# Optimization experiments

Measured on AMD Instinct MI355X. Metric: run time of the kernel, lower is better.

Reference implementation:

```python
import jax, jax.numpy as jnp
import numpy as np

HF = 14            # qubits (hidden_features)
SPECTRUM = 3       # spectrum_layer (data re-uploading blocks)
NSTEPS = 2         # N outer iterations
SEL_L = 3          # StronglyEntanglingLayers depth per block (weights1[..., 3, HF, 3])
DIM = 2 ** HF
BN_EPS = 1e-5

# wire 0 = most-significant bit (PennyLane default.qubit convention)
_bits = ((np.arange(DIM)[:, None] >> (HF - 1 - np.arange(HF))[None, :]) & 1)  # (DIM, HF)
Z_SIGNS = (1.0 - 2.0 * _bits).astype(np.float32)      # +1 for |0>, -1 for |1>
RZ_SIGNS = -Z_SIGNS                                    # (2b-1): RZ phase sign per wire
# CZ ring sign vectors for ranges r=1..SEL_L: (-1)^{sum_j b_j * b_{(j+r)%HF}}
_cz = []
for r in range(1, SEL_L + 1):
    parity = (_bits * _bits[:, (np.arange(HF) + r) % HF]).sum(axis=1) % 2
    _cz.append((1.0 - 2.0 * parity).astype(np.float32))
CZ_SIGNS = np.stack(_cz)  # (SEL_L, DIM)


def _rot_matrix(phi, theta, omega):
    # Rot = RZ(omega) @ RY(theta) @ RZ(phi)
    c = jnp.cos(theta / 2)
    s = jnp.sin(theta / 2)
    ep = jnp.exp(-0.5j * (phi + omega))
    em = jnp.exp(-0.5j * (phi - omega))
    return jnp.array([[ep * c, -jnp.conj(em) * s],
                      [em * s, jnp.conj(ep) * c]])


def _apply_1q(state, U, wire):
    # state: (b, 2^HF) complex; apply 2x2 U on `wire`
    b = state.shape[0]
    st = state.reshape(b, 2 ** wire, 2, -1)
    st = jnp.einsum('pq,bwqm->bwpm', U, st)
    return st.reshape(b, DIM)


def _run_circuit(x, w):
    # x: (b, HF) real RZ angles; w: (SPECTRUM, SEL_L, HF, 3)
    b = x.shape[0]
    state = jnp.zeros((b, DIM), jnp.complex64).at[:, 0].set(1.0)
    rz_diag = jnp.exp(0.5j * (x @ jnp.asarray(RZ_SIGNS).T))  # (b, DIM) complex64
    cz = jnp.asarray(CZ_SIGNS)
    for i in range(SPECTRUM):
        state = state * rz_diag                 # RZ(x_j) on every wire (diagonal)
        for l in range(SEL_L):
            for q in range(HF):
                state = _apply_1q(state, _rot_matrix(w[i, l, q, 0], w[i, l, q, 1], w[i, l, q, 2]), q)
            state = state * cz[l][None, :]      # CZ ring, range l+1 (diagonal +-1)
    probs = jnp.abs(state) ** 2
    return probs @ jnp.asarray(Z_SIGNS)          # <Z_j> per wire, (b, HF)


def setup_inputs() -> dict:
    key = jax.random.key(0)
    ks = jax.random.split(key, 6)
    b, c, w, h = 64, 1, 28, 28
    input_dim = c * w * h
    x = jax.random.normal(ks[0], (b, c, w, h), dtype=jnp.float32)
    w_down = jax.random.normal(ks[1], (HF, input_dim), dtype=jnp.float32) * (1.0 / np.sqrt(input_dim))
    b_down = jax.random.normal(ks[2], (HF,), dtype=jnp.float32) * 0.01
    bn_w = jnp.ones((HF,), jnp.float32)
    bn_b = jnp.zeros((HF,), jnp.float32)
    weights1 = jax.random.normal(ks[3], (NSTEPS, SPECTRUM, SEL_L, HF, 3), dtype=jnp.float32) * 0.4
    w_up = jax.random.normal(ks[4], (input_dim, HF), dtype=jnp.float32) * (1.0 / np.sqrt(HF))
    b_up = jax.random.normal(ks[5], (input_dim,), dtype=jnp.float32) * 0.01
    return {"x": x, "w_down": w_down, "b_down": b_down, "bn_w": bn_w, "bn_b": bn_b,
            "weights1": weights1, "w_up": w_up, "b_up": b_up}


def reference(x, w_down, b_down, bn_w, bn_b, weights1, w_up, b_up):
    b, c, w, h = x.shape
    xr = x.reshape(b, -1) @ w_down.T + b_down          # linear_down -> (b, HF)
    for n in range(NSTEPS):
        mu = xr.mean(axis=0)
        var = ((xr - mu) ** 2).mean(axis=0)            # BatchNorm1d, training-mode batch stats
        xr = (xr - mu) / jnp.sqrt(var + BN_EPS) * bn_w + bn_b
        xr = _run_circuit(xr, weights1[n])             # quantum circuit expvals -> (b, HF)
    out = xr @ w_up.T + b_up                           # linear_up
    return out.reshape(b, c, w, h)
```

## Files before the change

### kernel.cpp

```cpp
#include <hip/hip_runtime.h>
#include <math.h>

#define INV2PI 0.15915494309189535f

typedef _Float16 f16;
typedef _Float16 f16x8 __attribute__((ext_vector_type(8)));
typedef _Float16 f16x4 __attribute__((ext_vector_type(4)));
typedef float f32x16 __attribute__((ext_vector_type(16)));

#define Z16 {0.f,0.f,0.f,0.f,0.f,0.f,0.f,0.f,0.f,0.f,0.f,0.f,0.f,0.f,0.f,0.f}

#define WS_MATS 0
#define WS_TABS 262144
#define WS_RY1  266240
#define WS_XR   266304
#define WS_XR2  267200

__global__ void k_pre(const float* __restrict__ w1, float* __restrict__ ws)
{
    int blk = blockIdx.x, t = threadIdx.x;
    if (blk < 32) {
        int n = blk >> 4, rem = blk & 15, k = (rem >> 1) + 2, side = rem & 1;
        __shared__ float R[7][2][2];
        if (t < 7) {
            int wire = side ? (13 - t) : (6 - t);
            float th = w1[n*378 + (k-1)*42 + wire*3 + 1];
            float s, c; sincosf(0.5f*th, &s, &c);
            R[t][0][0] = c;  R[t][0][1] = -s;
            R[t][1][0] = s;  R[t][1][1] = c;
        }
        __syncthreads();
        f16* M = (f16*)ws + blk * 16384;
        for (int e = t; e < 16384; e += 256) {
            int tile = e >> 12, kk = (e >> 9) & 7, l = (e >> 3) & 63, j = e & 7;
            int row = tile*32 + (l & 31);
            int col = kk*16 + (l >> 5)*8 + j;
            float v = 1.f;
            #pragma unroll
            for (int bi = 0; bi < 7; ++bi) v *= R[bi][(row>>bi)&1][(col>>bi)&1];
            M[e] = (f16)v;
        }
    } else if (blk == 32) {
        for (int e = t; e < 4096; e += 256) {
            int n = e >> 11, r = e & 2047, k = (r >> 8) + 1;
            int r2 = r & 255, side = r2 >> 7, v = r2 & 127;
            float acc = 0.f;
            #pragma unroll
            for (int bi = 0; bi < 7; ++bi) {
                if ((v >> bi) & 1) {
                    int wire = side ? (13 - bi) : (6 - bi);
                    acc += (w1[n*378 + (k-1)*42 + wire*3 + 2]
                          + w1[n*378 + k*42     + wire*3 + 0]) * INV2PI;
                }
            }
            ws[WS_TABS + ((n*8 + (k-1))*2 + side)*128 + v] = acc;
        }
    } else {
        if (t < 28) {
            int n = t / 14, q = t % 14;
            float th = w1[n*378 + q*3 + 1];
            float s, c; sincosf(0.5f*th, &s, &c);
            ws[WS_RY1 + (n*14 + q)*2 + 0] = c;
            ws[WS_RY1 + (n*14 + q)*2 + 1] = s;
        }
    }
}

__global__ void k_down(const float* __restrict__ x, const float* __restrict__ wd,
                       const float* __restrict__ bd, float* __restrict__ xr)
{
    int row  = blockIdx.x;
    int wave = threadIdx.x >> 6;
    int lane = threadIdx.x & 63;
    const float* xrow = x + row * 784;
    for (int f = wave; f < 14; f += 4) {
        const float* wrow = wd + f * 784;
        float s = 0.f;
        for (int j = lane; j < 784; j += 64) s = fmaf(xrow[j], wrow[j], s);
        #pragma unroll
        for (int off = 32; off; off >>= 1) s += __shfl_xor(s, off);
        if (lane == 0) xr[row * 14 + f] = s + bd[f];
    }
}

template<int WHICH>
__global__ __launch_bounds__(1024)
void k_circuit(const f16* __restrict__ matsg, const float* __restrict__ tabsg,
               const float* __restrict__ ry1g, const float* __restrict__ xrin,
               float* __restrict__ xrout, const float* __restrict__ bnw,
               const float* __restrict__ bnb, const float* __restrict__ wu,
               const float* __restrict__ bu)
{
    __shared__ __align__(16) ushort SRe[16384];
    __shared__ __align__(16) ushort SIm[16384];
    __shared__ __align__(16) ushort IRe[16384];
    __shared__ __align__(16) ushort IIm[16384];
    __shared__ float2 ETAB[8][2][128];
    __shared__ float PA[128], PB[128];
    __shared__ float XR[896];
    __shared__ float XROW[14];
    __shared__ float RED[16][15];

    const int row = blockIdx.x, T = threadIdx.x;
    const int w = T >> 6, l = T & 63, lm = l & 31, hb = l >> 5;
    const int tm = w >> 2, tn = w & 3;
    const int mrow = tm*32 + lm, nn = tn*32 + lm;

    for (int i = T; i < 896; i += 1024) XR[i] = xrin[i];
    __syncthreads();
    if (T < 14) {
        float mu = 0.f;
        for (int r = 0; r < 64; ++r) mu += XR[r*14 + T];
        mu *= (1.f/64.f);
        float var = 0.f;
        for (int r = 0; r < 64; ++r) { float d = XR[r*14 + T] - mu; var += d*d; }
        var *= (1.f/64.f);
        float xb = (XR[row*14 + T] - mu) * rsqrtf(var + 1e-5f) * bnw[T] + bnb[T];
        XROW[T] = xb * INV2PI;
    }
    __syncthreads();
    for (int e = T; e < 2048; e += 1024) {
        int k0 = e >> 8, r2 = e & 255, side = r2 >> 7, v = r2 & 127;
        float val = tabsg[(k0*2 + side)*128 + v];
        if (k0 == 2 || k0 == 5) {
            #pragma unroll
            for (int bi = 0; bi < 7; ++bi)
                if ((v >> bi) & 1) val += XROW[side ? (13-bi) : (6-bi)];
        }
        float fr = __builtin_amdgcn_fractf(val);
        ETAB[k0][side][v] = make_float2(__builtin_amdgcn_cosf(fr),
                                        __builtin_amdgcn_sinf(fr));
    }
    if (T < 256) {
        int side = T >> 7, v = T & 127;
        float p = 1.f;
        #pragma unroll
        for (int bi = 0; bi < 7; ++bi) {
            int wire = side ? (13-bi) : (6-bi);
            p *= ((v >> bi) & 1) ? ry1g[wire*2 + 1] : ry1g[wire*2];
        }
        if (side) PB[v] = p; else PA[v] = p;
    }
    __syncthreads();
    {
        int a = T >> 3, b0 = (T & 7) << 4;
        float2 eA = ETAB[0][0][a];
        float pav = PA[a];
        #pragma unroll
        for (int g = 0; g < 2; ++g) {
            f16 hr[8], hm[8];
            #pragma unroll
            for (int u = 0; u < 8; ++u) {
                int b = b0 + g*8 + u;
                int d = (a << 7) | b;
                int rot = ((d >> 1) | (d << 13)) & 16383;
                float2 eB = ETAB[0][1][b];
                float zr = eA.x*eB.x - eA.y*eB.y;
                float zi = eA.x*eB.y + eA.y*eB.x;
                if (__popc(d & rot) & 1) { zr = -zr; zi = -zi; }
                float mg = pav * PB[b];
                hr[u] = (f16)(mg * zr);
                hm[u] = (f16)(mg * zi);
            }
            int hoff = ((a << 7) + b0 + g*8) ^ ((a & 15) << 3);
            f16x8 vr = {hr[0],hr[1],hr[2],hr[3],hr[4],hr[5],hr[6],hr[7]};
            f16x8 vi = {hm[0],hm[1],hm[2],hm[3],hm[4],hm[5],hm[6],hm[7]};
            *(f16x8*)((f16*)SRe + hoff) = vr;
            *(f16x8*)((f16*)SIm + hoff) = vi;
        }
    }
    __syncthreads();

    float tot = 0.f;
    float bs[14];
    #pragma unroll
    for (int i = 0; i < 14; ++i) bs[i] = 0.f;

    #pragma unroll 1
    for (int k = 2; k <= 9; ++k) {
        const int P = k & 1;
        const f16* M1 = matsg + ((k-2)*2 + (P ? 0 : 1)) * 16384;
        const f16* M2 = matsg + ((k-2)*2 + (P ? 1 : 0)) * 16384;
        f16x8 Bf[8];
        #pragma unroll
        for (int kk = 0; kk < 8; ++kk)
            Bf[kk] = *(const f16x8*)(M1 + (tn*8 + kk)*512 + l*8);
        f32x16 ar = Z16, ai = Z16;
        #pragma unroll
        for (int kk = 0; kk < 8; ++kk) {
            int c  = kk*16 + hb*8;
            int sa = ((mrow << 7) + c) ^ ((mrow & 15) << 3);
            f16x8 Ar = *(const f16x8*)((const f16*)SRe + sa);
            f16x8 Ai = *(const f16x8*)((const f16*)SIm + sa);
            ar = __builtin_amdgcn_mfma_f32_32x32x16_f16(Ar, Bf[kk], ar, 0,0,0);
            ai = __builtin_amdgcn_mfma_f32_32x32x16_f16(Ai, Bf[kk], ai, 0,0,0);
        }
        f16x8 Af[8];
        #pragma unroll
        for (int kk = 0; kk < 8; ++kk)
            Af[kk] = *(const f16x8*)(M2 + (tm*8 + kk)*512 + l*8);
        #pragma unroll
        for (int g = 0; g < 4; ++g) {
            int mb = tm*32 + g*8 + hb*4;
            int hoff = ((nn << 7) + mb) ^ ((nn & 15) << 3);
            f16x4 vr = {(f16)ar[g*4],(f16)ar[g*4+1],(f16)ar[g*4+2],(f16)ar[g*4+3]};
            f16x4 vi = {(f16)ai[g*4],(f16)ai[g*4+1],(f16)ai[g*4+2],(f16)ai[g*4+3]};
            *(f16x4*)((f16*)IRe + hoff) = vr;
            *(f16x4*)((f16*)IIm + hoff) = vi;
        }
        __syncthreads();
        f32x16 dr = Z16, di = Z16;
        #pragma unroll
        for (int kk = 0; kk < 8; ++kk) {
            int c  = kk*16 + hb*8;
            int s0 = ((nn << 7) + c) ^ ((nn & 15) << 3);
            f16x8 Br = *(const f16x8*)((const f16*)IRe + s0);
            f16x8 Bi = *(const f16x8*)((const f16*)IIm + s0);
            dr = __builtin_amdgcn_mfma_f32_32x32x16_f16(Af[kk], Br, dr, 0,0,0);
            di = __builtin_amdgcn_mfma_f32_32x32x16_f16(Af[kk], Bi, di, 0,0,0);
        }
        if (k < 9) {
            float2 eN = ETAB[k-1][P ? 0 : 1][nn];
            const int czr = ((k-1) % 3) + 1;
            f16 pr[16], pi[16];
            #pragma unroll
            for (int r = 0; r < 16; ++r) {
                int mloc = (r & 3) + 8*(r >> 2) + 4*hb;
                int mg = tm*32 + mloc;
                float2 eM = ETAB[k-1][P ? 1 : 0][mg];
                int d = P ? ((nn << 7) | mg) : ((mg << 7) | nn);
                int rot = ((d >> czr) | (d << (14 - czr))) & 16383;
                float zr = eM.x*eN.x - eM.y*eN.y;
                float zi = eM.x*eN.y + eM.y*eN.x;
                if (__popc(d & rot) & 1) { zr = -zr; zi = -zi; }
                float re = dr[r], im = di[r];
                pr[r] = (f16)(re*zr - im*zi);
                pi[r] = (f16)(re*zi + im*zr);
            }
            #pragma unroll
            for (int g = 0; g < 4; ++g) {
                int mb = tm*32 + g*8 + hb*4;
                int hoff = ((nn << 7) + mb) ^ ((nn & 15) << 3);
                f16x4 vr = {pr[g*4], pr[g*4+1], pr[g*4+2], pr[g*4+3]};
                f16x4 vi = {pi[g*4], pi[g*4+1], pi[g*4+2], pi[g*4+3]};
                *(f16x4*)((f16*)SRe + hoff) = vr;
                *(f16x4*)((f16*)SIm + hoff) = vi;
            }
        } else {
            float tp = 0.f, s0 = 0.f, s1v = 0.f, s3 = 0.f, s4 = 0.f;
            #pragma unroll
            for (int r = 0; r < 16; ++r) {
                float re = dr[r], im = di[r];
                float p = fmaf(re, re, im*im);
                tp += p;
                if (r & 1) s0  += p;
                if (r & 2) s1v += p;
                if (r & 4) s3  += p;
                if (r & 8) s4  += p;
            }
            tot += tp;
            bs[0] += s0; bs[1] += s1v; bs[3] += s3; bs[4] += s4;
            if (hb)     bs[2] += tp;
            if (tm & 1) bs[5] += tp;
            if (tm & 2) bs[6] += tp;
            #pragma unroll
            for (int i = 0; i < 7; ++i)
                if ((nn >> i) & 1) bs[7+i] += tp;
        }
        __syncthreads();
    }

    #pragma unroll
    for (int off = 32; off; off >>= 1) {
        tot += __shfl_xor(tot, off);
        #pragma unroll
        for (int i = 0; i < 14; ++i) bs[i] += __shfl_xor(bs[i], off);
    }
    if (l == 0) {
        #pragma unroll
        for (int i = 0; i < 14; ++i) RED[w][i] = bs[i];
        RED[w][14] = tot;
    }
    __syncthreads();
    if (T < 14) {
        float tt = 0.f, ss = 0.f;
        #pragma unroll
        for (int ww = 0; ww < 16; ++ww) { tt += RED[ww][14]; ss += RED[ww][13 - T]; }
        float val = tt - 2.f * ss;
        XROW[T] = val;
        if (WHICH == 0) xrout[row*14 + T] = val;
    }
    __syncthreads();
    if (WHICH == 1) {
        for (int j = T; j < 784; j += 1024) {
            float s = bu[j];
            #pragma unroll
            for (int f = 0; f < 14; ++f) s = fmaf(XROW[f], wu[j*14 + f], s);
            xrout[row*784 + j] = s;
        }
    }
}

extern "C" void kernel_launch(void* const* d_in, const int* in_sizes, int n_in,
                              void* d_out, int out_size, void* d_ws, size_t ws_size,
                              hipStream_t stream)
{
    const float* x  = (const float*)d_in[0];
    const float* wd = (const float*)d_in[1];
    const float* bd = (const float*)d_in[2];
    const float* bw = (const float*)d_in[3];
    const float* bb = (const float*)d_in[4];
    const float* w1 = (const float*)d_in[5];
    const float* wu = (const float*)d_in[6];
    const float* bu = (const float*)d_in[7];
    float* out = (float*)d_out;
    float* ws  = (float*)d_ws;

    hipLaunchKernelGGL(k_pre,  dim3(34), dim3(256), 0, stream, w1, ws);
    hipLaunchKernelGGL(k_down, dim3(64), dim3(256), 0, stream, x, wd, bd, ws + WS_XR);

    const f16* mats0 = (const f16*)ws;
    const f16* mats1 = (const f16*)ws + 262144;
    hipLaunchKernelGGL(k_circuit<0>, dim3(64), dim3(1024), 0, stream,
                       mats0, ws + WS_TABS, ws + WS_RY1,
                       ws + WS_XR, ws + WS_XR2, bw, bb, wu, bu);
    hipLaunchKernelGGL(k_circuit<1>, dim3(64), dim3(1024), 0, stream,
                       mats1, ws + WS_TABS + 2048, ws + WS_RY1 + 28,
                       ws + WS_XR2, out, bw, bb, wu, bu);
}
```

Measured before the change: 133.6 us.

## Prefetch next-stage B matrices, raise MFMA priority, and scope reduction registers

Loads the next stage's B-operand fragments from global memory during the CZ/phase epilogue of the current stage, so that latency overlaps with ALU work instead of stalling the next stage's first MFMA chain. It wraps the MFMA loops in s_setprio, moves the final-stage reduction state and shuffles into the last iteration, and processes the phase multiply in groups of four to shorten live ranges. It also adds a waves-per-EU hint to launch_bounds. Keeping Bf live across the loop adds register pressure, and the launch-bounds hint could force spills.

```diff
diff --git a/kernel.cpp b/kernel.cpp
--- a/kernel.cpp
+++ b/kernel.cpp
@@ -84,7 +84,7 @@
 }
 
 template<int WHICH>
-__global__ __launch_bounds__(1024)
+__global__ __launch_bounds__(1024, 4)
 void k_circuit(const f16* __restrict__ matsg, const float* __restrict__ tabsg,
                const float* __restrict__ ry1g, const float* __restrict__ xrin,
                float* __restrict__ xrout, const float* __restrict__ bnw,
@@ -171,21 +171,20 @@
     }
     __syncthreads();
 
-    float tot = 0.f;
-    float bs[14];
-    #pragma unroll
-    for (int i = 0; i < 14; ++i) bs[i] = 0.f;
+    f16x8 Bf[8], Af[8];
+    {
+        const f16* M1 = matsg + 1 * 16384;
+        #pragma unroll
+        for (int kk = 0; kk < 8; ++kk)
+            Bf[kk] = *(const f16x8*)(M1 + (tn*8 + kk)*512 + l*8);
+    }
 
     #pragma unroll 1
     for (int k = 2; k <= 9; ++k) {
         const int P = k & 1;
-        const f16* M1 = matsg + ((k-2)*2 + (P ? 0 : 1)) * 16384;
         const f16* M2 = matsg + ((k-2)*2 + (P ? 1 : 0)) * 16384;
-        f16x8 Bf[8];
-        #pragma unroll
-        for (int kk = 0; kk < 8; ++kk)
-            Bf[kk] = *(const f16x8*)(M1 + (tn*8 + kk)*512 + l*8);
         f32x16 ar = Z16, ai = Z16;
+        __builtin_amdgcn_s_setprio(1);
         #pragma unroll
         for (int kk = 0; kk < 8; ++kk) {
             int c  = kk*16 + hb*8;
@@ -195,7 +194,7 @@
             ar = __builtin_amdgcn_mfma_f32_32x32x16_f16(Ar, Bf[kk], ar, 0,0,0);
             ai = __builtin_amdgcn_mfma_f32_32x32x16_f16(Ai, Bf[kk], ai, 0,0,0);
         }
-        f16x8 Af[8];
+        __builtin_amdgcn_s_setprio(0);
         #pragma unroll
         for (int kk = 0; kk < 8; ++kk)
             Af[kk] = *(const f16x8*)(M2 + (tm*8 + kk)*512 + l*8);
@@ -210,6 +209,7 @@
         }
         __syncthreads();
         f32x16 dr = Z16, di = Z16;
+        __builtin_amdgcn_s_setprio(1);
         #pragma unroll
         for (int kk = 0; kk < 8; ++kk) {
             int c  = kk*16 + hb*8;
@@ -219,34 +219,47 @@
             dr = __builtin_amdgcn_mfma_f32_32x32x16_f16(Af[kk], Br, dr, 0,0,0);
             di = __builtin_amdgcn_mfma_f32_32x32x16_f16(Af[kk], Bi, di, 0,0,0);
         }
+        __builtin_amdgcn_s_setprio(0);
         if (k < 9) {
+            {
+                const int Pn = (k + 1) & 1;
+                const f16* M1n = matsg + ((k-1)*2 + (Pn ? 0 : 1)) * 16384;
+                #pragma unroll
+                for (int kk = 0; kk < 8; ++kk)
+                    Bf[kk] = *(const f16x8*)(M1n + (tn*8 + kk)*512 + l*8);
+            }
             float2 eN = ETAB[k-1][P ? 0 : 1][nn];
             const int czr = ((k-1) % 3) + 1;
-            f16 pr[16], pi[16];
-            #pragma unroll
-            for (int r = 0; r < 16; ++r) {
-                int mloc = (r & 3) + 8*(r >> 2) + 4*hb;
-                int mg = tm*32 + mloc;
-                float2 eM = ETAB[k-1][P ? 1 : 0][mg];
-                int d = P ? ((nn << 7) | mg) : ((mg << 7) | nn);
-                int rot = ((d >> czr) | (d << (14 - czr))) & 16383;
-                float zr = eM.x*eN.x - eM.y*eN.y;
-                float zi = eM.x*eN.y + eM.y*eN.x;
-                if (__popc(d & rot) & 1) { zr = -zr; zi = -zi; }
-                float re = dr[r], im = di[r];
-                pr[r] = (f16)(re*zr - im*zi);
-                pi[r] = (f16)(re*zi + im*zr);
-            }
             #pragma unroll
             for (int g = 0; g < 4; ++g) {
+                float prf[4], pif[4];
+                #pragma unroll
+                for (int u = 0; u < 4; ++u) {
+                    int r = g*4 + u;
+                    int mloc = (r & 3) + 8*(r >> 2) + 4*hb;
+                    int mg = tm*32 + mloc;
+                    float2 eM = ETAB[k-1][P ? 1 : 0][mg];
+                    int d = P ? ((nn << 7) | mg) : ((mg << 7) | nn);
+                    int rot = ((d >> czr) | (d << (14 - czr))) & 16383;
+                    float zr = eM.x*eN.x - eM.y*eN.y;
+                    float zi = eM.x*eN.y + eM.y*eN.x;
+                    if (__popc(d & rot) & 1) { zr = -zr; zi = -zi; }
+                    float re = dr[r], im = di[r];
+                    prf[u] = re*zr - im*zi;
+                    pif[u] = re*zi + im*zr;
+                }
                 int mb = tm*32 + g*8 + hb*4;
                 int hoff = ((nn << 7) + mb) ^ ((nn & 15) << 3);
-                f16x4 vr = {pr[g*4], pr[g*4+1], pr[g*4+2], pr[g*4+3]};
-                f16x4 vi = {pi[g*4], pi[g*4+1], pi[g*4+2], pi[g*4+3]};
+                f16x4 vr = {(f16)prf[0],(f16)prf[1],(f16)prf[2],(f16)prf[3]};
+                f16x4 vi = {(f16)pif[0],(f16)pif[1],(f16)pif[2],(f16)pif[3]};
                 *(f16x4*)((f16*)SRe + hoff) = vr;
                 *(f16x4*)((f16*)SIm + hoff) = vi;
             }
         } else {
+            float tot = 0.f;
+            float bs[14];
+            #pragma unroll
+            for (int i = 0; i < 14; ++i) bs[i] = 0.f;
             float tp = 0.f, s0 = 0.f, s1v = 0.f, s3 = 0.f, s4 = 0.f;
             #pragma unroll
             for (int r = 0; r < 16; ++r) {
@@ -266,22 +279,21 @@
             #pragma unroll
             for (int i = 0; i < 7; ++i)
                 if ((nn >> i) & 1) bs[7+i] += tp;
+            #pragma unroll
+            for (int off = 32; off; off >>= 1) {
+                tot += __shfl_xor(tot, off);
+                #pragma unroll
+                for (int i = 0; i < 14; ++i) bs[i] += __shfl_xor(bs[i], off);
+            }
+            if (l == 0) {
+                #pragma unroll
+                for (int i = 0; i < 14; ++i) RED[w][i] = bs[i];
+                RED[w][14] = tot;
+            }
         }
         __syncthreads();
     }
 
-    #pragma unroll
-    for (int off = 32; off; off >>= 1) {
-        tot += __shfl_xor(tot, off);
-        #pragma unroll
-        for (int i = 0; i < 14; ++i) bs[i] += __shfl_xor(bs[i], off);
-    }
-    if (l == 0) {
-        #pragma unroll
-        for (int i = 0; i < 14; ++i) RED[w][i] = bs[i];
-        RED[w][14] = tot;
-    }
-    __syncthreads();
     if (T < 14) {
         float tt = 0.f, ss = 0.f;
         #pragma unroll
```

Measured after the change: 153.6 us. +15.0%, slower.
